# Optimization experiments

Measured on AMD Instinct MI355X. Metric: run time of the kernel, lower is better.

The kernel has to match this reference:

```python
import jax, jax.numpy as jnp
from jax import lax
import numpy as np

B, C, L, HOP = 16, 64, 16384, 256
KS = 3        # LVC / conv kernel size
DIL = 3       # static Conv1d dilation (init arg)
KL = L // HOP # kernel_length (number of conditioning frames)


def setup_inputs() -> dict:
    key = jax.random.key(0)
    k0, k1, k2, k3 = jax.random.split(key, 4)
    return {
        "hidden_states": jax.random.normal(k0, (B, C, L), jnp.float32),
        "kernel": jax.random.normal(k1, (B, C, 2 * C, KS, KL), jnp.float32) * 0.05,
        "bias": jax.random.normal(k2, (B, 2 * C, KL), jnp.float32) * 0.05,
        "conv_w": jax.random.normal(k3, (C, C, KS), jnp.float32) * 0.05,
        "conv_b": jnp.zeros((C,), jnp.float32),
        "hop_size": HOP,
    }


def _lvc(x, kernel, bias, hop_size):
    # location-variable convolution; forward() uses dilation=1 here
    b, c, length = x.shape
    _, _, out_ch, ksize, klen = kernel.shape
    pad = (ksize - 1) // 2
    xp = jnp.pad(x, ((0, 0), (0, 0), (pad, pad)))
    # sliding windows of size ksize, stride 1 -> (b, c, length, ksize)
    win = jnp.stack([xp[:, :, i:i + length] for i in range(ksize)], axis=-1)
    # split time into (kernel_length, hop_size) frames
    win = win.reshape(b, c, klen, hop_size, ksize)
    # per-frame conv kernel contraction
    o = jnp.einsum('bilsk,biokl->bols', win, kernel)  # (b, out_ch, klen, hop)
    o = o + bias[:, :, :, None]
    return o.reshape(b, out_ch, klen * hop_size)


def reference(hidden_states, kernel, bias, conv_w, conv_b, hop_size):
    slope = 0.2
    pad = DIL * (KS - 1) // 2
    residual = hidden_states
    h = jax.nn.leaky_relu(hidden_states, slope)
    h = lax.conv_general_dilated(
        h, conv_w, window_strides=(1,), padding=[(pad, pad)],
        rhs_dilation=(DIL,), dimension_numbers=('NCH', 'OIH', 'NCH'))
    h = h + conv_b[None, :, None]
    h = jax.nn.leaky_relu(h, slope)
    h = _lvc(h, kernel, bias, hop_size)
    c = residual.shape[1]
    h = jax.nn.sigmoid(h[:, :c, :]) * jnp.tanh(h[:, c:, :])  # GLU gate
    return residual + h
```

## Files before the change

### kernel.cpp

```cpp
#include <hip/hip_runtime.h>
#include <hip/hip_bf16.h>

#define TB 256

typedef __attribute__((ext_vector_type(8))) short short8;
typedef __attribute__((ext_vector_type(4))) unsigned int uint4v;
typedef __attribute__((ext_vector_type(4))) float f32x4;

#define KTF_BYTES 50331648ull
#define WS_NEED   (KTF_BYTES + 24576ull)

static __device__ __forceinline__ float lrelu(float v){ return v > 0.f ? v : 0.2f*v; }

static __device__ __forceinline__ unsigned int pack2(float lo, float hi){
    __hip_bfloat162 h = __float22bfloat162_rn(float2{lo, hi});
    unsigned int r;
    __builtin_memcpy(&r, &h, 4);
    return r;
}

static __device__ __forceinline__ float bf2f(unsigned int u16v){
    return __uint_as_float(u16v << 16);
}

static __device__ __forceinline__ float glu_gate(float a, float t){
    float u = __expf(-a);
    float v = __expf(2.0f * t);
    float den = (1.0f + u) * (v + 1.0f);
    return (v - 1.0f) * __builtin_amdgcn_rcpf(den);
}


__global__ __launch_bounds__(256, 4)
void ktf_transpose(const float* __restrict__ kern, unsigned int* __restrict__ ktf)
{
    __shared__ unsigned int tl32[128 * 65];
    const int tid = threadIdx.x;
    const int blk = blockIdx.x;
    const int k   = blk % 3;
    const int ci2 = (blk / 3) % 32;
    const int b   = blk / 96;
    const int kk  = k*2 + (ci2 >> 4);
    const int hi  = (ci2 >> 2) & 3;
    const int jp  = ci2 & 3;

    const float* src0 = kern + (size_t)b*1572864 + (size_t)ci2*49152 + k*64;
    #pragma unroll
    for (int it = 0; it < 8; ++it) {
        int p = tid + it*TB;
        int oc = p >> 4, fq = p & 15;
        const float* s = src0 + oc*192 + fq*4;
        float4 v0 = *(const float4*)(s);
        float4 v1 = *(const float4*)(s + 24576);
        unsigned int* d = tl32 + oc*65 + fq*4;
        d[0] = pack2(v0.x, v1.x);
        d[1] = pack2(v0.y, v1.y);
        d[2] = pack2(v0.z, v1.z);
        d[3] = pack2(v0.w, v1.w);
    }
    __syncthreads();

    const int l = tid & 63, wvv = tid >> 6;
    const int c = (kk*4 + jp)*4 + hi;
    const int oc0 = 2*l;
    const int slot0 = (oc0 < 64)
        ? ((oc0 >> 3)*16 + ((oc0 & 7) >> 1)*4)
        : (((oc0 - 64) >> 3)*16 + (((oc0 - 64) & 7) >> 1)*4 + 2);
    unsigned int* dst = ktf + (size_t)(b*96 + c)*8192 + slot0;
    const int f0 = wvv*16;
    #pragma unroll
    for (int fi = 0; fi < 16; ++fi) {
        int f = f0 + fi;
        uint2 v;
        v.x = tl32[(oc0    )*65 + f];
        v.y = tl32[(oc0 + 1)*65 + f];
        *(uint2*)(dst + f*128) = v;
    }
}

__global__ __launch_bounds__(256, 4)
void wf_prep(const float* __restrict__ conv_w, unsigned int* __restrict__ wf)
{
    int u = blockIdx.x*TB + threadIdx.x;
    int ln = u & 63, mt = (u >> 6) & 3, jp = (u >> 8) & 3, kk = u >> 10;
    int lo = ln & 15, hi = ln >> 4;
    int m  = mt*16 + lo;
    int k  = kk >> 1, ci = (kk & 1)*32 + hi*8 + jp*2;
    float a0 = conv_w[m*192 + ci*3 + k];
    float a1 = conv_w[m*192 + (ci + 1)*3 + k];
    wf[u] = pack2(a0, a1);
}

#define LDS_XT1  18432
#define LDS_HT   36864
#define LDS_BIAS 55296

#define X_LOAD(TS_, XV_)                                                      \
    do {                                                                      \
        const int ts_ = (TS_);                                                \
        const bool inter_ = (ts_ >= 0) & (ts_ + 143 < 16384);                 \
        if (inter_) {                                                         \
            _Pragma("unroll")                                                 \
            for (int it = 0; it < 2; ++it)                                    \
                if (it == 0 || ln < 8) {                                      \
                    int t = ts_ + 2*ln + it*128;                              \
                    _Pragma("unroll")                                         \
                    for (int j = 0; j < 8; ++j)                               \
                        XV_[it][j] = *(const float2*)(xb + j*16384 + t);      \
                }                                                             \
        } else {                                                              \
            _Pragma("unroll")                                                 \
            for (int it = 0; it < 2; ++it)                                    \
                if (it == 0 || ln < 8) {                                      \
                    int t = ts_ + 2*ln + it*128;                              \
                    _Pragma("unroll")                                         \
                    for (int j = 0; j < 8; ++j) {                             \
                        float a0_ = ((unsigned)t       < 16384u) ? xb[j*16384 + t    ] : 0.f; \
                        float a1_ = ((unsigned)(t + 1) < 16384u) ? xb[j*16384 + t + 1] : 0.f; \
                        XV_[it][j] = make_float2(a0_, a1_);                   \
                    }                                                         \
                }                                                             \
        }                                                                     \
    } while (0)

#define X_STORE(XTB_, XV_)                                                    \
    do {                                                                      \
        _Pragma("unroll")                                                     \
        for (int it = 0; it < 2; ++it)                                        \
            if (it == 0 || ln < 8) {                                          \
                int p0 = 2*ln + it*128;                                       \
                unsigned int w0_[4], w1_[4];                                  \
                _Pragma("unroll")                                             \
                for (int jq = 0; jq < 4; ++jq) {                              \
                    float2 e0_ = XV_[it][2*jq], e1_ = XV_[it][2*jq + 1];      \
                    w0_[jq] = pack2(lrelu(e0_.x), lrelu(e1_.x));              \
                    w1_[jq] = pack2(lrelu(e0_.y), lrelu(e1_.y));              \
                }                                                             \
                int a0_ = (XTB_) + (( p0     *128 + wv*16) ^ (( p0      & 7) << 4)); \
                int a1_ = (XTB_) + (((p0 + 1)*128 + wv*16) ^ (((p0 + 1) & 7) << 4)); \
                *(uint4*)(lds + a0_) = make_uint4(w0_[0], w0_[1], w0_[2], w0_[3]); \
                *(uint4*)(lds + a1_) = make_uint4(w1_[0], w1_[1], w1_[2], w1_[3]); \
            }                                                                 \
    } while (0)

#define B_PHASE(XTB_, TB_)                                                    \
    do {                                                                      \
        uint4v aw_[6];                                                        \
        _Pragma("unroll")                                                     \
        for (int kk = 0; kk < 6; ++kk) {                                      \
            int w0_ = kk*1024 + mt*64 + ln;                                   \
            aw_[kk].x = wf[w0_      ]; aw_[kk].y = wf[w0_ + 256];             \
            aw_[kk].z = wf[w0_ + 512]; aw_[kk].w = wf[w0_ + 768];             \
        }                                                                     \
        float4 cb4_ = *(const float4*)(conv_b + mt*16 + hi*4);                \
        const int n0_  = nth ? 5 : 0;                                         \
        const int cnt_ = nth ? 4 : 5;                                         \
        int bqa_[6];                                                          \
        _Pragma("unroll")                                                     \
        for (int kk = 0; kk < 6; ++kk) {                                      \
            int row_ = n0_*16 + lo + 3*(kk >> 1) + 1;                         \
            int cib_ = (kk & 1)*32 + hi*8;                                    \
            bqa_[kk] = (XTB_) + ((row_*128 + cib_*2) ^ ((row_ & 7) << 4));    \
        }                                                                     \
        int hta_ = LDS_HT + (((n0_*16 + lo)*128 + (mt*16 + hi*4)*2) ^ ((lo & 7) << 4)); \
        int pos_ = (TB_) + n0_*16 + lo - 8;                                   \
        _Pragma("unroll 1")                                                   \
        for (int i = 0; i < cnt_; ++i) {                                      \
            f32x4 acc_ = {0.f, 0.f, 0.f, 0.f};                                \
            __builtin_amdgcn_s_setprio(1);                                    \
            _Pragma("unroll")                                                 \
            for (int kk = 0; kk < 6; ++kk) {                                  \
                short8 bq_ = *(const short8*)(lds + bqa_[kk]);                \
                acc_ = __builtin_amdgcn_mfma_f32_16x16x32_bf16(               \
                        __builtin_bit_cast(short8, aw_[kk]), bq_, acc_, 0, 0, 0); \
            }                                                                 \
            __builtin_amdgcn_s_setprio(0);                                    \
            bool valid_ = (unsigned)pos_ < 16384u;                            \
            unsigned int h01_ = valid_ ? pack2(lrelu(acc_[0] + cb4_.x), lrelu(acc_[1] + cb4_.y)) : 0u; \
            unsigned int h23_ = valid_ ? pack2(lrelu(acc_[2] + cb4_.z), lrelu(acc_[3] + cb4_.w)) : 0u; \
            unsigned int* d_ = (unsigned int*)(lds + hta_);                   \
            d_[0] = h01_; d_[1] = h23_;                                       \
            _Pragma("unroll")                                                 \
            for (int kk = 0; kk < 6; ++kk) bqa_[kk] += 2048;                  \
            hta_ += 2048; pos_ += 16;                                         \
        }                                                                     \
    } while (0)

#define C_PHASE(XTB_, TB_)                                                    \
    do {                                                                      \
        int bqa_[6];                                                          \
        _Pragma("unroll")                                                     \
        for (int kk = 0; kk < 6; ++kk) {                                      \
            int row_ = lo + 7 + (kk >> 1);                                    \
            int cib_ = (kk & 1)*32 + hi*8;                                    \
            bqa_[kk] = LDS_HT + ((row_*128 + cib_*2) ^ ((row_ & 7) << 4));    \
        }                                                                     \
        const int q_  = lo + 12;                                              \
        int ra_ = (XTB_) + ((q_*128 + ch2*2) ^ ((q_ & 7) << 4));              \
        float* ob_ = out + ((size_t)b*64 + ch2)*16384 + (TB_) + lo;           \
        _Pragma("unroll 1")                                                   \
        for (int i = 0; i < 8; ++i) {                                         \
            f32x4 acc_ = {0.f, 0.f, 0.f, 0.f};                                \
            __builtin_amdgcn_s_setprio(1);                                    \
            _Pragma("unroll")                                                 \
            for (int kk = 0; kk < 6; ++kk) {                                  \
                short8 bq_ = *(const short8*)(lds + bqa_[kk]);                \
                acc_ = __builtin_amdgcn_mfma_f32_16x16x32_bf16(               \
                        __builtin_bit_cast(short8, am[kk]), bq_, acc_, 0, 0, 0); \
            }                                                                 \
            __builtin_amdgcn_s_setprio(0);                                    \
            unsigned int rvc_ = *(const unsigned int*)(lds + ra_);            \
            float h0_ = bf2f(rvc_ & 0xFFFFu), h1_ = bf2f(rvc_ >> 16);         \
            float g0_ = glu_gate(acc_[0] + bs0, acc_[2] + bt0);               \
            float g1_ = glu_gate(acc_[1] + bs1, acc_[3] + bt1);               \
            ob_[(size_t)i*16]         = fminf(h0_, 5.0f*h0_) + g0_;           \
            ob_[16384 + (size_t)i*16] = fminf(h1_, 5.0f*h1_) + g1_;           \
            _Pragma("unroll")                                                 \
            for (int kk = 0; kk < 6; ++kk) bqa_[kk] += 2048;                  \
            ra_ += 2048;                                                      \
        }                                                                     \
    } while (0)

__global__ __launch_bounds__(512, 4)
void fused_kernel(const float* __restrict__ x,
                  const float* __restrict__ bias,
                  const float* __restrict__ conv_b,
                  const unsigned int* __restrict__ ktf,
                  const unsigned int* __restrict__ wf,
                  float* __restrict__ out)
{
    __shared__ char lds[55808];
    float* bias_lds = (float*)(lds + LDS_BIAS);

    const int tid = threadIdx.x;
    const int blk = blockIdx.x;
    const int b = blk >> 6, f = blk & 63;
    const int t0 = f << 8;
    const int ln = tid & 63, wv = tid >> 6;
    const int lo = ln & 15, hi = ln >> 4;
    const int mt = wv & 3, nth = wv >> 2;

    const float* xb = x + ((size_t)b*64 + wv*8) * 16384;
    float2 xv[2][8];

    X_LOAD(t0 - 12, xv);
    __builtin_amdgcn_sched_barrier(0);

    uint4v am[6];
    {
        const unsigned int* kp = ktf + (size_t)b*786432 + hi*8192 + f*128 + wv*16 + lo;
        #pragma unroll
        for (int kk = 0; kk < 6; ++kk) {
            int o = kk*131072;
            am[kk].x = kp[o        ]; am[kk].y = kp[o + 32768];
            am[kk].z = kp[o + 65536]; am[kk].w = kp[o + 98304];
        }
    }
    if (tid < 128) bias_lds[tid] = bias[(size_t)b*8192 + tid*64 + f];
    __builtin_amdgcn_sched_barrier(0);

    X_STORE(0, xv);
    __syncthreads();

    const int ch2 = wv*8 + 2*hi;
    const float bs0 = bias_lds[ch2],      bs1 = bias_lds[ch2 + 1];
    const float bt0 = bias_lds[ch2 + 64], bt1 = bias_lds[ch2 + 65];

    X_LOAD(t0 + 116, xv);
    __builtin_amdgcn_sched_barrier(0);

    B_PHASE(0, t0);
    __syncthreads();
    C_PHASE(0, t0);
    X_STORE(LDS_XT1, xv);
    __syncthreads();

    B_PHASE(LDS_XT1, t0 + 128);
    __syncthreads();
    C_PHASE(LDS_XT1, t0 + 128);
}

extern "C" void kernel_launch(void* const* d_in, const int* in_sizes, int n_in,
                              void* d_out, int out_size, void* d_ws, size_t ws_size,
                              hipStream_t stream)
{
    const float* x      = (const float*)d_in[0];
    const float* kern   = (const float*)d_in[1];
    const float* bias   = (const float*)d_in[2];
    const float* conv_b = (const float*)d_in[4];
    float* out = (float*)d_out;

    if (ws_size < WS_NEED) return;

    unsigned int* ktf = (unsigned int*)d_ws;
    unsigned int* wf  = (unsigned int*)((char*)d_ws + KTF_BYTES);

    wf_prep      <<<dim3(24),   dim3(TB), 0, stream>>>((const float*)d_in[3], wf);
    ktf_transpose<<<dim3(1536), dim3(TB), 0, stream>>>(kern, ktf);
    fused_kernel <<<dim3(1024), dim3(512), 0, stream>>>(x, bias, conv_b, ktf, wf, out);
    (void)in_sizes; (void)n_in; (void)out_size;
}
```

Before: 96.92 us.

## Drop double-buffered x tile to shrink LDS and raise occupancy

Result: slower. 119.9 us (+23.7%).

```diff
diff --git a/kernel.cpp b/kernel.cpp
--- a/kernel.cpp
+++ b/kernel.cpp
@@ -91,9 +91,8 @@
     wf[u] = pack2(a0, a1);
 }
 
-#define LDS_XT1  18432
-#define LDS_HT   36864
-#define LDS_BIAS 55296
+#define LDS_HT   18432
+#define LDS_BIAS 36864
 
 #define X_LOAD(TS_, XV_)                                                      \
     do {                                                                      \
@@ -123,7 +122,7 @@
         }                                                                     \
     } while (0)
 
-#define X_STORE(XTB_, XV_)                                                    \
+#define X_STORE(XV_)                                                          \
     do {                                                                      \
         _Pragma("unroll")                                                     \
         for (int it = 0; it < 2; ++it)                                        \
@@ -136,14 +135,14 @@
                     w0_[jq] = pack2(lrelu(e0_.x), lrelu(e1_.x));              \
                     w1_[jq] = pack2(lrelu(e0_.y), lrelu(e1_.y));              \
                 }                                                             \
-                int a0_ = (XTB_) + (( p0     *128 + wv*16) ^ (( p0      & 7) << 4)); \
-                int a1_ = (XTB_) + (((p0 + 1)*128 + wv*16) ^ (((p0 + 1) & 7) << 4)); \
+                int a0_ = ( p0     *128 + wv*16) ^ (( p0      & 7) << 4);     \
+                int a1_ = ((p0 + 1)*128 + wv*16) ^ (((p0 + 1) & 7) << 4);     \
                 *(uint4*)(lds + a0_) = make_uint4(w0_[0], w0_[1], w0_[2], w0_[3]); \
                 *(uint4*)(lds + a1_) = make_uint4(w1_[0], w1_[1], w1_[2], w1_[3]); \
             }                                                                 \
     } while (0)
 
-#define B_PHASE(XTB_, TB_)                                                    \
+#define B_PHASE(TB_)                                                          \
     do {                                                                      \
         uint4v aw_[6];                                                        \
         _Pragma("unroll")                                                     \
@@ -160,7 +159,7 @@
         for (int kk = 0; kk < 6; ++kk) {                                      \
             int row_ = n0_*16 + lo + 3*(kk >> 1) + 1;                         \
             int cib_ = (kk & 1)*32 + hi*8;                                    \
-            bqa_[kk] = (XTB_) + ((row_*128 + cib_*2) ^ ((row_ & 7) << 4));    \
+            bqa_[kk] = (row_*128 + cib_*2) ^ ((row_ & 7) << 4);               \
         }                                                                     \
         int hta_ = LDS_HT + (((n0_*16 + lo)*128 + (mt*16 + hi*4)*2) ^ ((lo & 7) << 4)); \
         int pos_ = (TB_) + n0_*16 + lo - 8;                                   \
@@ -186,7 +185,7 @@
         }                                                                     \
     } while (0)
 
-#define C_PHASE(XTB_, TB_)                                                    \
+#define C_PHASE(TB_)                                                          \
     do {                                                                      \
         int bqa_[6];                                                          \
         _Pragma("unroll")                                                     \
@@ -196,7 +195,7 @@
             bqa_[kk] = LDS_HT + ((row_*128 + cib_*2) ^ ((row_ & 7) << 4));    \
         }                                                                     \
         const int q_  = lo + 12;                                              \
-        int ra_ = (XTB_) + ((q_*128 + ch2*2) ^ ((q_ & 7) << 4));              \
+        int ra_ = (q_*128 + ch2*2) ^ ((q_ & 7) << 4);                         \
         float* ob_ = out + ((size_t)b*64 + ch2)*16384 + (TB_) + lo;           \
         _Pragma("unroll 1")                                                   \
         for (int i = 0; i < 8; ++i) {                                         \
@@ -221,7 +220,7 @@
         }                                                                     \
     } while (0)
 
-__global__ __launch_bounds__(512, 4)
+__global__ __launch_bounds__(512, 5)
 void fused_kernel(const float* __restrict__ x,
                   const float* __restrict__ bias,
                   const float* __restrict__ conv_b,
@@ -229,7 +228,7 @@
                   const unsigned int* __restrict__ wf,
                   float* __restrict__ out)
 {
-    __shared__ char lds[55808];
+    __shared__ char lds[37376];
     float* bias_lds = (float*)(lds + LDS_BIAS);
 
     const int tid = threadIdx.x;
@@ -241,11 +240,15 @@
     const int mt = wv & 3, nth = wv >> 2;
 
     const float* xb = x + ((size_t)b*64 + wv*8) * 16384;
-    float2 xv[2][8];
-
-    X_LOAD(t0 - 12, xv);
-    __builtin_amdgcn_sched_barrier(0);
-
+
+    {
+        float2 xv[2][8];
+        X_LOAD(t0 - 12, xv);
+        __builtin_amdgcn_sched_barrier(0);
+        if (tid < 128) bias_lds[tid] = bias[(size_t)b*8192 + tid*64 + f];
+        __builtin_amdgcn_sched_barrier(0);
+        X_STORE(xv);
+    }
     uint4v am[6];
     {
         const unsigned int* kp = ktf + (size_t)b*786432 + hi*8192 + f*128 + wv*16 + lo;
@@ -256,28 +259,27 @@
             am[kk].z = kp[o + 65536]; am[kk].w = kp[o + 98304];
         }
     }
-    if (tid < 128) bias_lds[tid] = bias[(size_t)b*8192 + tid*64 + f];
-    __builtin_amdgcn_sched_barrier(0);
-
-    X_STORE(0, xv);
     __syncthreads();
 
     const int ch2 = wv*8 + 2*hi;
     const float bs0 = bias_lds[ch2],      bs1 = bias_lds[ch2 + 1];
     const float bt0 = bias_lds[ch2 + 64], bt1 = bias_lds[ch2 + 65];
 
-    X_LOAD(t0 + 116, xv);
-    __builtin_amdgcn_sched_barrier(0);
-
-    B_PHASE(0, t0);
-    __syncthreads();
-    C_PHASE(0, t0);
-    X_STORE(LDS_XT1, xv);
-    __syncthreads();
-
-    B_PHASE(LDS_XT1, t0 + 128);
-    __syncthreads();
-    C_PHASE(LDS_XT1, t0 + 128);
+    B_PHASE(t0);
+    __syncthreads();
+    C_PHASE(t0);
+    __syncthreads();
+
+    {
+        float2 xv[2][8];
+        X_LOAD(t0 + 116, xv);
+        X_STORE(xv);
+    }
+    __syncthreads();
+
+    B_PHASE(t0 + 128);
+    __syncthreads();
+    C_PHASE(t0 + 128);
 }
 
 extern "C" void kernel_launch(void* const* d_in, const int* in_sizes, int n_in,
```
